# Kernel optimization log

Measured on AMD Instinct MI355X. Metric: run time of the kernel, lower is better.

Reference implementation:

```python
import jax, jax.numpy as jnp
import numpy as np

N_NODES = 100000
N_EDGES = 1600000


def setup_inputs() -> dict:
    key = jax.random.key(0)
    ks = jax.random.split(key, 8)
    x = jax.random.normal(ks[0], (N_NODES, 100), dtype=jnp.float32)
    edge_index = jax.random.randint(ks[1], (2, N_EDGES), 0, N_NODES, dtype=jnp.int64)
    edge_weight = jax.random.uniform(ks[2], (N_EDGES,), dtype=jnp.float32)
    # params (kaiming-ish scale)
    W_conv = jax.random.normal(ks[3], (100, 32), dtype=jnp.float32) * (1.0 / np.sqrt(100))
    b_conv = jnp.zeros((32,), jnp.float32)
    W1 = jax.random.normal(ks[4], (32, 16), dtype=jnp.float32) * (1.0 / np.sqrt(32))
    b1 = jnp.zeros((16,), jnp.float32)
    W2 = jax.random.normal(ks[5], (16, 8), dtype=jnp.float32) * (1.0 / np.sqrt(16))
    b2 = jnp.zeros((8,), jnp.float32)
    W3 = jax.random.normal(ks[6], (8, 10), dtype=jnp.float32) * (1.0 / np.sqrt(8))
    b3 = jnp.zeros((10,), jnp.float32)
    return {"x": x, "edge_index": edge_index, "edge_weight": edge_weight,
            "W_conv": W_conv, "b_conv": b_conv, "W1": W1, "b1": b1,
            "W2": W2, "b2": b2, "W3": W3, "b3": b3}


def gcn_conv(x, edge_index, W, b, n_nodes):
    # PyG GCNConv: add self-loops, symmetric deg^-0.5 normalization, unit edge weights
    loop = jnp.arange(n_nodes, dtype=edge_index.dtype)
    src = jnp.concatenate([edge_index[0], loop])
    dst = jnp.concatenate([edge_index[1], loop])
    deg = jax.ops.segment_sum(jnp.ones_like(dst, dtype=x.dtype), dst,
                              num_segments=n_nodes)
    dinv = jax.lax.rsqrt(jnp.maximum(deg, 1e-12))  # deg >= 1 due to self-loops
    norm = dinv[src] * dinv[dst]                   # [E+N]
    h = x @ W                                      # [N, 32]
    msg = h[src] * norm[:, None]                   # gather + scale
    out = jax.ops.segment_sum(msg, dst, num_segments=n_nodes)  # scatter-add
    return out + b


def reference(x, edge_index, edge_weight, W_conv, b_conv, W1, b1, W2, b2, W3, b3):
    # edge_weight is accepted by the original forward but never used (conv1(x, edge_index))
    n_nodes = x.shape[0]
    h = jax.nn.relu(gcn_conv(x, edge_index, W_conv, b_conv, n_nodes))
    # F.dropout with training=False (eval) is identity
    h = jax.nn.relu(h @ W1 + b1)
    h = jax.nn.relu(h @ W2 + b2)
    h = h @ W3 + b3
    return jax.nn.log_softmax(h, axis=1)
```

## Files before the change

### kernel.cpp

```cpp
#include <hip/hip_runtime.h>
#include <hip/hip_fp16.h>
#include <math.h>

#define N_NODES 100000
#define N_EDGES 1600000
#define F_IN 100
#define F_H 32

#define BKT_SHIFT 7
#define BKT_C 128
#define NBK 782
#define BKT_CAP 2560
#define BF_B 1024
#define BF_EPT 8
#define BF_TILE 8192
#define BF_GRID 196
#define AG_B 512
#define AG_CAP BKT_CAP
#define AG_EPT 5

#define XW_B 256
#define XW_R 128
#define XW_S2 51

__global__ __launch_bounds__(BF_B) void binfill_kernel(
        const int* __restrict__ src, const int* __restrict__ dst,
        int* __restrict__ gcursor, unsigned* __restrict__ packed) {
    __shared__ int cnt[NBK];
    __shared__ int lbase[NBK];
    __shared__ int gbase[NBK];
    __shared__ int wsums[16];
    __shared__ unsigned stage[BF_TILE];
    __shared__ unsigned short stageB[BF_TILE];
    __shared__ int tot;
    int t = threadIdx.x;
    long base = (long)blockIdx.x * BF_TILE;
    for (int i = t; i < NBK; i += BF_B) cnt[i] = 0;
    __syncthreads();
    int myb[BF_EPT]; int mypos[BF_EPT]; unsigned mypk[BF_EPT];
#pragma unroll
    for (int k = 0; k < BF_EPT; k++) {
        long e = base + t + (long)k * BF_B;
        myb[k] = -1;
        if (e < N_EDGES) {
            int d = dst[e];
            int sI = src[e];
            int b = d >> BKT_SHIFT;
            myb[k] = b;
            mypk[k] = (unsigned)sI | ((unsigned)(d & (BKT_C - 1)) << 17);
            mypos[k] = atomicAdd(&cnt[b], 1);
        }
    }
    __syncthreads();
    if (t < NBK && cnt[t] > 0)
        gbase[t] = t * BKT_CAP + atomicAdd(&gcursor[t], cnt[t]);
    int lane = t & 63, w = t >> 6;
    int v = (t < NBK) ? cnt[t] : 0;
    int sc = v;
#pragma unroll
    for (int off = 1; off < 64; off <<= 1) {
        int x = __shfl_up(sc, off, 64);
        if (lane >= off) sc += x;
    }
    if (lane == 63) wsums[w] = sc;
    __syncthreads();
    int pre = 0;
#pragma unroll
    for (int u = 0; u < 16; u++) pre += (u < w) ? wsums[u] : 0;
    int incl = sc + pre;
    if (t < NBK) lbase[t] = incl - v;
    if (t == BF_B - 1) tot = incl;
    __syncthreads();
#pragma unroll
    for (int k = 0; k < BF_EPT; k++) {
        if (myb[k] >= 0) {
            int p = lbase[myb[k]] + mypos[k];
            stage[p] = mypk[k];
            stageB[p] = (unsigned short)myb[k];
        }
    }
    __syncthreads();
    int T = tot;
    for (int i = t; i < T; i += BF_B) {
        int b = stageB[i];
        packed[gbase[b] + (i - lbase[b])] = stage[i];
    }
}

__global__ __launch_bounds__(XW_B) void degxw_kernel(
        const int* __restrict__ blen, const unsigned* __restrict__ packed,
        const float* __restrict__ x, const float* __restrict__ W,
        float* __restrict__ dinv, __half* __restrict__ h2) {
    __shared__ __half2 xs[XW_R * XW_S2];
    __shared__ int cnt[BKT_C];
    __shared__ float sdinv[BKT_C];
    int t = threadIdx.x;
    int b = blockIdx.x;
    if (t < BKT_C) cnt[t] = 0;
    __syncthreads();
    int beg = b * BKT_CAP, end = beg + blen[b];
    for (int i = beg + t; i < end; i += XW_B)
        atomicAdd(&cnt[(packed[i] >> 17) & (BKT_C - 1)], 1);
    __syncthreads();
    int rbase = b << BKT_SHIFT;
    int rows = min(XW_R, N_NODES - rbase);
    if (t < BKT_C) {
        float dv = rsqrtf((float)cnt[t] + 1.0f);
        sdinv[t] = dv;
        if (t < rows) dinv[rbase + t] = dv;
    }
    int total = rows * F_IN;
    const float4* gx4 = (const float4*)(x + (long)rbase * F_IN);
    for (int i4 = t; i4 < (total >> 2); i4 += XW_B) {
        float4 v = gx4[i4];
        int i = i4 << 2;
        int r = i / F_IN;
        int k = i - r * F_IN;
        __half2* p = xs + r * XW_S2 + (k >> 1);
        p[0] = __floats2half2_rn(v.x, v.y);
        p[1] = __floats2half2_rn(v.z, v.w);
    }
    __syncthreads();
    int r = t & (XW_R - 1);
    int colh16 = __builtin_amdgcn_readfirstlane((t >> 7) << 4);
    if (r < rows) {
        const float* Wp = W + colh16;
        float acc[16];
#pragma unroll
        for (int j = 0; j < 16; j++) acc[j] = 0.f;
        const __half2* xr = xs + r * XW_S2;
#pragma unroll 5
        for (int k2 = 0; k2 < F_IN / 2; k2++) {
            float2 xv = __half22float2(xr[k2]);
#pragma unroll
            for (int j = 0; j < 16; j++)
                acc[j] = fmaf(xv.y, Wp[(2 * k2 + 1) * F_H + j],
                              fmaf(xv.x, Wp[(2 * k2) * F_H + j], acc[j]));
        }
        float dv = sdinv[r];
        __half2 o[8];
#pragma unroll
        for (int j = 0; j < 8; j++)
            o[j] = __halves2half2(__float2half(acc[2 * j] * dv),
                                  __float2half(acc[2 * j + 1] * dv));
        float4* dst4 = (float4*)(h2 + (long)(rbase + r) * F_H + colh16);
        dst4[0] = ((float4*)o)[0];
        dst4[1] = ((float4*)o)[1];
    }
}

__global__ __launch_bounds__(AG_B) void agg_kernel(
        const int* __restrict__ blen, const unsigned* __restrict__ packed,
        const __half* __restrict__ h2, const float* __restrict__ dinv,
        const float* __restrict__ bc,
        const float* __restrict__ W1, const float* __restrict__ b1,
        const float* __restrict__ W2, const float* __restrict__ b2,
        const float* __restrict__ W3, const float* __restrict__ b3,
        float* __restrict__ out) {
    __shared__ float accL[BKT_C * 33];
    __shared__ int esrc[AG_CAP];
    __shared__ int cnt[BKT_C];
    __shared__ int lbase[BKT_C];
    __shared__ int wsum;
    __shared__ float sbc[32], sW1[512], sb1[16], sW2[128], sb2[8], sW3[80], sb3[10];
    int t = threadIdx.x;
    if (t < 32) sbc[t] = bc[t];
    if (t < 512) sW1[t] = W1[t];
    if (t < 16) sb1[t] = b1[t];
    if (t < 128) sW2[t] = W2[t];
    if (t < 8) sb2[t] = b2[t];
    if (t < 80) sW3[t] = W3[t];
    if (t < 10) sb3[t] = b3[t];

    int b = blockIdx.x;
    int beg = b * BKT_CAP;
    int cnum = blen[b];
    if (t < BKT_C) cnt[t] = 0;
    __syncthreads();
    unsigned pk[AG_EPT]; int pos[AG_EPT];
#pragma unroll
    for (int k = 0; k < AG_EPT; k++) {
        int idx = t + k * AG_B;
        pk[k] = 0xFFFFFFFFu;
        if (idx < cnum) {
            unsigned p = packed[beg + idx];
            pk[k] = p;
            pos[k] = atomicAdd(&cnt[(p >> 17) & (BKT_C - 1)], 1);
        }
    }
    __syncthreads();
    {
        int lane = t & 63;
        int v = 0;
        if (t < BKT_C) {
            v = cnt[t];
#pragma unroll
            for (int off = 1; off < 64; off <<= 1) {
                int xx = __shfl_up(v, off, 64);
                if (lane >= off) v += xx;
            }
            if (t == 63) wsum = v;
        }
        __syncthreads();
        if (t < BKT_C) {
            if (t >= 64) v += wsum;
            lbase[t] = v;
        }
    }
    __syncthreads();
#pragma unroll
    for (int k = 0; k < AG_EPT; k++) {
        if (pk[k] != 0xFFFFFFFFu) {
            int lid = (pk[k] >> 17) & (BKT_C - 1);
            esrc[lbase[lid] - cnt[lid] + pos[k]] = (int)(pk[k] & 0x1FFFF);
        }
    }
    __syncthreads();
    {
        int g = t >> 2, l = t & 3;
        const float4* h2o = (const float4*)h2;
        int e = lbase[g] - cnt[g];
        int eend = lbase[g];
        float a0 = 0.f, a1 = 0.f, a2 = 0.f, a3 = 0.f;
        float a4 = 0.f, a5 = 0.f, a6 = 0.f, a7 = 0.f;
        for (; e + 8 <= eend; e += 8) {
            int s0 = esrc[e], s1 = esrc[e+1], s2 = esrc[e+2], s3 = esrc[e+3];
            int s4 = esrc[e+4], s5 = esrc[e+5], s6 = esrc[e+6], s7 = esrc[e+7];
            float4 q0 = h2o[s0 * 4 + l];
            float4 q1 = h2o[s1 * 4 + l];
            float4 q2 = h2o[s2 * 4 + l];
            float4 q3 = h2o[s3 * 4 + l];
            float4 q4 = h2o[s4 * 4 + l];
            float4 q5 = h2o[s5 * 4 + l];
            float4 q6 = h2o[s6 * 4 + l];
            float4 q7 = h2o[s7 * 4 + l];
#pragma unroll
            for (int u = 0; u < 8; u++) {
                float4 q = (u == 0) ? q0 : (u == 1) ? q1 : (u == 2) ? q2 :
                           (u == 3) ? q3 : (u == 4) ? q4 : (u == 5) ? q5 :
                           (u == 6) ? q6 : q7;
                const __half2* hp = (const __half2*)&q;
                float2 f0 = __half22float2(hp[0]);
                float2 f1 = __half22float2(hp[1]);
                float2 f2 = __half22float2(hp[2]);
                float2 f3 = __half22float2(hp[3]);
                a0 += f0.x; a1 += f0.y; a2 += f1.x; a3 += f1.y;
                a4 += f2.x; a5 += f2.y; a6 += f3.x; a7 += f3.y;
            }
        }
        for (; e < eend; e++) {
            float4 q = h2o[esrc[e] * 4 + l];
            const __half2* hp = (const __half2*)&q;
            float2 f0 = __half22float2(hp[0]);
            float2 f1 = __half22float2(hp[1]);
            float2 f2 = __half22float2(hp[2]);
            float2 f3 = __half22float2(hp[3]);
            a0 += f0.x; a1 += f0.y; a2 += f1.x; a3 += f1.y;
            a4 += f2.x; a5 += f2.y; a6 += f3.x; a7 += f3.y;
        }
        float* ap = accL + g * 33 + 8 * l;
        ap[0] = a0; ap[1] = a1; ap[2] = a2; ap[3] = a3;
        ap[4] = a4; ap[5] = a5; ap[6] = a6; ap[7] = a7;
    }
    __syncthreads();

    int n = (b << BKT_SHIFT) + t;
    if (t < BKT_C && n < N_NODES) {
        float dv = dinv[n];
        const __half2* h2v = (const __half2*)h2;
        float a[32];
#pragma unroll
        for (int q = 0; q < 16; q++) {
            float2 hv = __half22float2(h2v[n * 16 + q]);
            a[2*q]   = fmaxf((accL[t * 33 + 2*q]   + hv.x) * dv + sbc[2*q],   0.f);
            a[2*q+1] = fmaxf((accL[t * 33 + 2*q+1] + hv.y) * dv + sbc[2*q+1], 0.f);
        }
        float t1[16];
#pragma unroll
        for (int j = 0; j < 16; j++) {
            float s = sb1[j];
            for (int k = 0; k < 32; k++) s += a[k] * sW1[k * 16 + j];
            t1[j] = fmaxf(s, 0.f);
        }
        float t2[8];
#pragma unroll
        for (int j = 0; j < 8; j++) {
            float s = sb2[j];
            for (int k = 0; k < 16; k++) s += t1[k] * sW2[k * 8 + j];
            t2[j] = fmaxf(s, 0.f);
        }
        float t3[10];
#pragma unroll
        for (int j = 0; j < 10; j++) {
            float s = sb3[j];
            for (int k = 0; k < 8; k++) s += t2[k] * sW3[k * 10 + j];
            t3[j] = s;
        }
        float m = t3[0];
#pragma unroll
        for (int j = 1; j < 10; j++) m = fmaxf(m, t3[j]);
        float se = 0.f;
#pragma unroll
        for (int j = 0; j < 10; j++) se += expf(t3[j] - m);
        float lse = logf(se) + m;
        float* op = out + (long)n * 10;
#pragma unroll
        for (int j = 0; j < 10; j++) op[j] = t3[j] - lse;
    }
}

extern "C" void kernel_launch(void* const* d_in, const int* in_sizes, int n_in,
                              void* d_out, int out_size, void* d_ws, size_t ws_size,
                              hipStream_t stream) {
    const float* x  = (const float*)d_in[0];
    const int*   ei = (const int*)d_in[1];
    const float* Wc = (const float*)d_in[3];
    const float* bc = (const float*)d_in[4];
    const float* W1 = (const float*)d_in[5];
    const float* b1 = (const float*)d_in[6];
    const float* W2 = (const float*)d_in[7];
    const float* b2 = (const float*)d_in[8];
    const float* W3 = (const float*)d_in[9];
    const float* b3 = (const float*)d_in[10];
    float* out = (float*)d_out;

    __half*   h2      = (__half*)d_ws;
    unsigned* packed  = (unsigned*)((char*)d_ws + (long)N_NODES * F_H * 2);
    float*    dinv    = (float*)(packed + (long)NBK * BKT_CAP);
    int*      gcursor = (int*)(dinv + N_NODES);

    const int* srcp = ei;
    const int* dstp = ei + N_EDGES;

    hipMemsetAsync(gcursor, 0, NBK * sizeof(int), stream);
    binfill_kernel<<<BF_GRID, BF_B, 0, stream>>>(srcp, dstp, gcursor, packed);
    degxw_kernel<<<NBK, XW_B, 0, stream>>>(gcursor, packed, x, Wc, dinv, h2);
    agg_kernel<<<NBK, AG_B, 0, stream>>>(gcursor, packed, h2, dinv, bc, W1, b1, W2, b2,
                                         W3, b3, out);
}
```

Measured before the change: 175.0 us.

## Fuse edge binning with XW matmul, defer source-degree normalization to aggregation

Merges the binning kernel and the X·W kernel into one launch whose blocks are split by role, so the matmul no longer has to wait for binning. Because dinv is not known when h is produced, degree is counted with global float atomics during binning and h is stored unnormalized. The aggregation kernel then applies rsqrt(deg+1) per gathered source edge. This removes one launch and the serialization between the two stages, at the cost of 1.6M global atomics and an extra random degree gather plus rsqrt per edge.

Result: slower. 247.1 us (+41.2%).

```diff
diff --git a/kernel.cpp b/kernel.cpp
--- a/kernel.cpp
+++ b/kernel.cpp
@@ -11,147 +11,137 @@
 #define BKT_C 128
 #define NBK 782
 #define BKT_CAP 2560
+
 #define BF_B 1024
 #define BF_EPT 8
 #define BF_TILE 8192
 #define BF_GRID 196
+
+#define XW_ROWS 256
+#define XW_S2 51
+#define XW_GRID 391
+
+#define FUSE_GRID (BF_GRID + XW_GRID)
+#define SM_BYTES 58624
+
 #define AG_B 512
 #define AG_CAP BKT_CAP
 #define AG_EPT 5
 
-#define XW_B 256
-#define XW_R 128
-#define XW_S2 51
-
-__global__ __launch_bounds__(BF_B) void binfill_kernel(
+__global__ __launch_bounds__(BF_B, 8) void fused1_kernel(
         const int* __restrict__ src, const int* __restrict__ dst,
-        int* __restrict__ gcursor, unsigned* __restrict__ packed) {
-    __shared__ int cnt[NBK];
-    __shared__ int lbase[NBK];
-    __shared__ int gbase[NBK];
-    __shared__ int wsums[16];
-    __shared__ unsigned stage[BF_TILE];
-    __shared__ unsigned short stageB[BF_TILE];
-    __shared__ int tot;
+        int* __restrict__ gcursor, unsigned* __restrict__ packed,
+        float* __restrict__ degf,
+        const float* __restrict__ x, const float* __restrict__ W,
+        __half* __restrict__ h2) {
+    __shared__ char smraw[SM_BYTES] __attribute__((aligned(16)));
     int t = threadIdx.x;
-    long base = (long)blockIdx.x * BF_TILE;
-    for (int i = t; i < NBK; i += BF_B) cnt[i] = 0;
-    __syncthreads();
-    int myb[BF_EPT]; int mypos[BF_EPT]; unsigned mypk[BF_EPT];
-#pragma unroll
-    for (int k = 0; k < BF_EPT; k++) {
-        long e = base + t + (long)k * BF_B;
-        myb[k] = -1;
-        if (e < N_EDGES) {
-            int d = dst[e];
-            int sI = src[e];
-            int b = d >> BKT_SHIFT;
-            myb[k] = b;
-            mypk[k] = (unsigned)sI | ((unsigned)(d & (BKT_C - 1)) << 17);
-            mypos[k] = atomicAdd(&cnt[b], 1);
-        }
-    }
-    __syncthreads();
-    if (t < NBK && cnt[t] > 0)
-        gbase[t] = t * BKT_CAP + atomicAdd(&gcursor[t], cnt[t]);
-    int lane = t & 63, w = t >> 6;
-    int v = (t < NBK) ? cnt[t] : 0;
-    int sc = v;
-#pragma unroll
-    for (int off = 1; off < 64; off <<= 1) {
-        int x = __shfl_up(sc, off, 64);
-        if (lane >= off) sc += x;
-    }
-    if (lane == 63) wsums[w] = sc;
-    __syncthreads();
-    int pre = 0;
-#pragma unroll
-    for (int u = 0; u < 16; u++) pre += (u < w) ? wsums[u] : 0;
-    int incl = sc + pre;
-    if (t < NBK) lbase[t] = incl - v;
-    if (t == BF_B - 1) tot = incl;
-    __syncthreads();
-#pragma unroll
-    for (int k = 0; k < BF_EPT; k++) {
-        if (myb[k] >= 0) {
-            int p = lbase[myb[k]] + mypos[k];
-            stage[p] = mypk[k];
-            stageB[p] = (unsigned short)myb[k];
-        }
-    }
-    __syncthreads();
-    int T = tot;
-    for (int i = t; i < T; i += BF_B) {
-        int b = stageB[i];
-        packed[gbase[b] + (i - lbase[b])] = stage[i];
-    }
-}
-
-__global__ __launch_bounds__(XW_B) void degxw_kernel(
-        const int* __restrict__ blen, const unsigned* __restrict__ packed,
-        const float* __restrict__ x, const float* __restrict__ W,
-        float* __restrict__ dinv, __half* __restrict__ h2) {
-    __shared__ __half2 xs[XW_R * XW_S2];
-    __shared__ int cnt[BKT_C];
-    __shared__ float sdinv[BKT_C];
-    int t = threadIdx.x;
-    int b = blockIdx.x;
-    if (t < BKT_C) cnt[t] = 0;
-    __syncthreads();
-    int beg = b * BKT_CAP, end = beg + blen[b];
-    for (int i = beg + t; i < end; i += XW_B)
-        atomicAdd(&cnt[(packed[i] >> 17) & (BKT_C - 1)], 1);
-    __syncthreads();
-    int rbase = b << BKT_SHIFT;
-    int rows = min(XW_R, N_NODES - rbase);
-    if (t < BKT_C) {
-        float dv = rsqrtf((float)cnt[t] + 1.0f);
-        sdinv[t] = dv;
-        if (t < rows) dinv[rbase + t] = dv;
-    }
-    int total = rows * F_IN;
-    const float4* gx4 = (const float4*)(x + (long)rbase * F_IN);
-    for (int i4 = t; i4 < (total >> 2); i4 += XW_B) {
-        float4 v = gx4[i4];
-        int i = i4 << 2;
-        int r = i / F_IN;
-        int k = i - r * F_IN;
-        __half2* p = xs + r * XW_S2 + (k >> 1);
-        p[0] = __floats2half2_rn(v.x, v.y);
-        p[1] = __floats2half2_rn(v.z, v.w);
-    }
-    __syncthreads();
-    int r = t & (XW_R - 1);
-    int colh16 = __builtin_amdgcn_readfirstlane((t >> 7) << 4);
-    if (r < rows) {
-        const float* Wp = W + colh16;
-        float acc[16];
-#pragma unroll
-        for (int j = 0; j < 16; j++) acc[j] = 0.f;
-        const __half2* xr = xs + r * XW_S2;
+    if (blockIdx.x < BF_GRID) {
+        int* cnt = (int*)smraw;
+        int* lbase = cnt + NBK;
+        int* gbase = lbase + NBK;
+        int* wsums = gbase + NBK;
+        int* ptot = wsums + 16;
+        unsigned* stage = (unsigned*)(ptot + 1);
+        unsigned short* stageB = (unsigned short*)(stage + BF_TILE);
+        long base = (long)blockIdx.x * BF_TILE;
+        for (int i = t; i < NBK; i += BF_B) cnt[i] = 0;
+        __syncthreads();
+        int myb[BF_EPT]; int mypos[BF_EPT]; unsigned mypk[BF_EPT];
+#pragma unroll
+        for (int k = 0; k < BF_EPT; k++) {
+            long e = base + t + (long)k * BF_B;
+            myb[k] = -1;
+            if (e < N_EDGES) {
+                int d = dst[e];
+                int sI = src[e];
+                int b = d >> BKT_SHIFT;
+                myb[k] = b;
+                mypk[k] = (unsigned)sI | ((unsigned)(d & (BKT_C - 1)) << 17);
+                mypos[k] = atomicAdd(&cnt[b], 1);
+                atomicAdd(&degf[d], 1.0f);
+            }
+        }
+        __syncthreads();
+        if (t < NBK && cnt[t] > 0)
+            gbase[t] = t * BKT_CAP + atomicAdd(&gcursor[t], cnt[t]);
+        int lane = t & 63, w = t >> 6;
+        int v = (t < NBK) ? cnt[t] : 0;
+        int sc = v;
+#pragma unroll
+        for (int off = 1; off < 64; off <<= 1) {
+            int xx = __shfl_up(sc, off, 64);
+            if (lane >= off) sc += xx;
+        }
+        if (lane == 63) wsums[w] = sc;
+        __syncthreads();
+        int pre = 0;
+#pragma unroll
+        for (int u = 0; u < 16; u++) pre += (u < w) ? wsums[u] : 0;
+        int incl = sc + pre;
+        if (t < NBK) lbase[t] = incl - v;
+        if (t == BF_B - 1) ptot[0] = incl;
+        __syncthreads();
+#pragma unroll
+        for (int k = 0; k < BF_EPT; k++) {
+            if (myb[k] >= 0) {
+                int p = lbase[myb[k]] + mypos[k];
+                stage[p] = mypk[k];
+                stageB[p] = (unsigned short)myb[k];
+            }
+        }
+        __syncthreads();
+        int T = ptot[0];
+        for (int i = t; i < T; i += BF_B) {
+            int b = stageB[i];
+            packed[gbase[b] + (i - lbase[b])] = stage[i];
+        }
+    } else {
+        __half2* xs = (__half2*)smraw;
+        int rbase = (blockIdx.x - BF_GRID) * XW_ROWS;
+        int rows = min(XW_ROWS, N_NODES - rbase);
+        int total = rows * F_IN;
+        const float4* gx4 = (const float4*)(x + (long)rbase * F_IN);
+        for (int i4 = t; i4 < (total >> 2); i4 += BF_B) {
+            float4 v = gx4[i4];
+            int i = i4 << 2;
+            int r = i / F_IN;
+            int k = i - r * F_IN;
+            __half2* p = xs + r * XW_S2 + (k >> 1);
+            p[0] = __floats2half2_rn(v.x, v.y);
+            p[1] = __floats2half2_rn(v.z, v.w);
+        }
+        __syncthreads();
+        int r = t & (XW_ROWS - 1);
+        int colbase = __builtin_amdgcn_readfirstlane((t >> 8) << 3);
+        if (r < rows) {
+            const float* Wp = W + colbase;
+            float acc[8];
+#pragma unroll
+            for (int j = 0; j < 8; j++) acc[j] = 0.f;
+            const __half2* xr = xs + r * XW_S2;
 #pragma unroll 5
-        for (int k2 = 0; k2 < F_IN / 2; k2++) {
-            float2 xv = __half22float2(xr[k2]);
-#pragma unroll
-            for (int j = 0; j < 16; j++)
-                acc[j] = fmaf(xv.y, Wp[(2 * k2 + 1) * F_H + j],
-                              fmaf(xv.x, Wp[(2 * k2) * F_H + j], acc[j]));
-        }
-        float dv = sdinv[r];
-        __half2 o[8];
-#pragma unroll
-        for (int j = 0; j < 8; j++)
-            o[j] = __halves2half2(__float2half(acc[2 * j] * dv),
-                                  __float2half(acc[2 * j + 1] * dv));
-        float4* dst4 = (float4*)(h2 + (long)(rbase + r) * F_H + colh16);
-        dst4[0] = ((float4*)o)[0];
-        dst4[1] = ((float4*)o)[1];
+            for (int k2 = 0; k2 < F_IN / 2; k2++) {
+                float2 xv = __half22float2(xr[k2]);
+#pragma unroll
+                for (int j = 0; j < 8; j++)
+                    acc[j] = fmaf(xv.y, Wp[(2 * k2 + 1) * F_H + j],
+                                  fmaf(xv.x, Wp[(2 * k2) * F_H + j], acc[j]));
+            }
+            __half2 o[4];
+#pragma unroll
+            for (int j = 0; j < 4; j++)
+                o[j] = __halves2half2(__float2half(acc[2 * j]),
+                                      __float2half(acc[2 * j + 1]));
+            float4* dst4 = (float4*)(h2 + (long)(rbase + r) * F_H + colbase);
+            dst4[0] = ((float4*)o)[0];
+        }
     }
 }
 
 __global__ __launch_bounds__(AG_B) void agg_kernel(
         const int* __restrict__ blen, const unsigned* __restrict__ packed,
-        const __half* __restrict__ h2, const float* __restrict__ dinv,
+        const __half* __restrict__ h2, const float* __restrict__ degf,
         const float* __restrict__ bc,
         const float* __restrict__ W1, const float* __restrict__ b1,
         const float* __restrict__ W2, const float* __restrict__ b2,
@@ -234,29 +224,46 @@
             float4 q5 = h2o[s5 * 4 + l];
             float4 q6 = h2o[s6 * 4 + l];
             float4 q7 = h2o[s7 * 4 + l];
+            float d0 = rsqrtf(degf[s0] + 1.0f);
+            float d1 = rsqrtf(degf[s1] + 1.0f);
+            float d2 = rsqrtf(degf[s2] + 1.0f);
+            float d3 = rsqrtf(degf[s3] + 1.0f);
+            float d4 = rsqrtf(degf[s4] + 1.0f);
+            float d5 = rsqrtf(degf[s5] + 1.0f);
+            float d6 = rsqrtf(degf[s6] + 1.0f);
+            float d7 = rsqrtf(degf[s7] + 1.0f);
 #pragma unroll
             for (int u = 0; u < 8; u++) {
                 float4 q = (u == 0) ? q0 : (u == 1) ? q1 : (u == 2) ? q2 :
                            (u == 3) ? q3 : (u == 4) ? q4 : (u == 5) ? q5 :
                            (u == 6) ? q6 : q7;
+                float dd = (u == 0) ? d0 : (u == 1) ? d1 : (u == 2) ? d2 :
+                           (u == 3) ? d3 : (u == 4) ? d4 : (u == 5) ? d5 :
+                           (u == 6) ? d6 : d7;
                 const __half2* hp = (const __half2*)&q;
                 float2 f0 = __half22float2(hp[0]);
                 float2 f1 = __half22float2(hp[1]);
                 float2 f2 = __half22float2(hp[2]);
                 float2 f3 = __half22float2(hp[3]);
-                a0 += f0.x; a1 += f0.y; a2 += f1.x; a3 += f1.y;
-                a4 += f2.x; a5 += f2.y; a6 += f3.x; a7 += f3.y;
+                a0 = fmaf(f0.x, dd, a0); a1 = fmaf(f0.y, dd, a1);
+                a2 = fmaf(f1.x, dd, a2); a3 = fmaf(f1.y, dd, a3);
+                a4 = fmaf(f2.x, dd, a4); a5 = fmaf(f2.y, dd, a5);
+                a6 = fmaf(f3.x, dd, a6); a7 = fmaf(f3.y, dd, a7);
             }
         }
         for (; e < eend; e++) {
-            float4 q = h2o[esrc[e] * 4 + l];
+            int s = esrc[e];
+            float4 q = h2o[s * 4 + l];
+            float dd = rsqrtf(degf[s] + 1.0f);
             const __half2* hp = (const __half2*)&q;
             float2 f0 = __half22float2(hp[0]);
             float2 f1 = __half22float2(hp[1]);
             float2 f2 = __half22float2(hp[2]);
             float2 f3 = __half22float2(hp[3]);
-            a0 += f0.x; a1 += f0.y; a2 += f1.x; a3 += f1.y;
-            a4 += f2.x; a5 += f2.y; a6 += f3.x; a7 += f3.y;
+            a0 = fmaf(f0.x, dd, a0); a1 = fmaf(f0.y, dd, a1);
+            a2 = fmaf(f1.x, dd, a2); a3 = fmaf(f1.y, dd, a3);
+            a4 = fmaf(f2.x, dd, a4); a5 = fmaf(f2.y, dd, a5);
+            a6 = fmaf(f3.x, dd, a6); a7 = fmaf(f3.y, dd, a7);
         }
         float* ap = accL + g * 33 + 8 * l;
         ap[0] = a0; ap[1] = a1; ap[2] = a2; ap[3] = a3;
@@ -266,14 +273,14 @@
 
     int n = (b << BKT_SHIFT) + t;
     if (t < BKT_C && n < N_NODES) {
-        float dv = dinv[n];
+        float dv = rsqrtf((float)cnt[t] + 1.0f);
         const __half2* h2v = (const __half2*)h2;
         float a[32];
 #pragma unroll
         for (int q = 0; q < 16; q++) {
             float2 hv = __half22float2(h2v[n * 16 + q]);
-            a[2*q]   = fmaxf((accL[t * 33 + 2*q]   + hv.x) * dv + sbc[2*q],   0.f);
-            a[2*q+1] = fmaxf((accL[t * 33 + 2*q+1] + hv.y) * dv + sbc[2*q+1], 0.f);
+            a[2*q]   = fmaxf((accL[t * 33 + 2*q]   + hv.x * dv) * dv + sbc[2*q],   0.f);
+            a[2*q+1] = fmaxf((accL[t * 33 + 2*q+1] + hv.y * dv) * dv + sbc[2*q+1], 0.f);
         }
         float t1[16];
 #pragma unroll
@@ -326,15 +333,15 @@
 
     __half*   h2      = (__half*)d_ws;
     unsigned* packed  = (unsigned*)((char*)d_ws + (long)N_NODES * F_H * 2);
-    float*    dinv    = (float*)(packed + (long)NBK * BKT_CAP);
-    int*      gcursor = (int*)(dinv + N_NODES);
+    float*    degf    = (float*)(packed + (long)NBK * BKT_CAP);
+    int*      gcursor = (int*)(degf + N_NODES);
 
     const int* srcp = ei;
     const int* dstp = ei + N_EDGES;
 
-    hipMemsetAsync(gcursor, 0, NBK * sizeof(int), stream);
-    binfill_kernel<<<BF_GRID, BF_B, 0, stream>>>(srcp, dstp, gcursor, packed);
-    degxw_kernel<<<NBK, XW_B, 0, stream>>>(gcursor, packed, x, Wc, dinv, h2);
-    agg_kernel<<<NBK, AG_B, 0, stream>>>(gcursor, packed, h2, dinv, bc, W1, b1, W2, b2,
-                                         W3, b3, out);
+    hipMemsetAsync(degf, 0, (N_NODES + NBK) * sizeof(float), stream);
+    fused1_kernel<<<FUSE_GRID, BF_B, 0, stream>>>(srcp, dstp, gcursor, packed,
+                                                  degf, x, Wc, h2);
+    agg_kernel<<<NBK, AG_B, 0, stream>>>(gcursor, packed, h2, degf, bc, W1, b1,
+                                         W2, b2, W3, b3, out);
 }
```
